# Kernel tuning notes

Measured on AMD Instinct MI355X. Metric: run time of the kernel, lower is better.

Reference implementation:

```python
import jax, jax.numpy as jnp
import numpy as np


def setup_inputs() -> dict:
    key = jax.random.key(0)
    ks = jax.random.split(key, 8)
    B, T, C = 4, 1024, 1024
    s = 1.0 / np.sqrt(C)
    return {
        "q": jax.random.normal(ks[0], (B, T, C), jnp.float32),
        "k": jax.random.normal(ks[1], (B, T, C), jnp.float32),
        "v": jax.random.normal(ks[2], (B, T, C), jnp.float32),
        "Wq": jax.random.normal(ks[3], (C, C), jnp.float32) * s,
        "Wk": jax.random.normal(ks[4], (C, C), jnp.float32) * s,
        "Wv": jax.random.normal(ks[5], (C, C), jnp.float32) * s,
        "Wp": jax.random.normal(ks[6], (C, C), jnp.float32) * s,
        "bp": jnp.zeros((C,), jnp.float32),
        "n_head": 16,
        "kernel_size": 16,
    }


def reference(q, k, v, Wq, Wk, Wv, Wp, bp, n_head, kernel_size):
    B, T, C = q.shape
    H = n_head
    D = C // H

    def split_heads(x, W):
        # nn.Linear applies x @ W.T
        return (x @ W.T).reshape(B, T, H, D).transpose(0, 2, 1, 3)  # (B,H,T,D)

    qp = split_heads(q, Wq)
    kp = split_heads(k, Wk)
    vp = split_heads(v, Wv)

    # Faithful to the torch double loop: wei[b,h,i,j] = sum over feature dims
    # d in [max(0, j-ks), min(T, j+ks)) (clipped to [0,D)) of qp[b,h,i,d]*kp[b,h,i,d] / sqrt(D).
    # Both windows index sequence position i; the window slides over the head_dim axis.
    p = qp * kp / jnp.sqrt(jnp.asarray(D, qp.dtype))          # (B,H,T,D)
    cs = jnp.cumsum(p, axis=-1)
    cs = jnp.concatenate([jnp.zeros(cs.shape[:-1] + (1,), cs.dtype), cs], axis=-1)  # (B,H,T,D+1)
    j = jnp.arange(T)
    start = jnp.clip(j - kernel_size, 0, D)                   # (T,)
    end = jnp.clip(jnp.minimum(j + kernel_size, T), 0, D)     # (T,)
    wei = cs[..., end] - cs[..., start]                       # (B,H,T,T): windowed partial dot of row i

    attn = jax.nn.softmax(wei, axis=-1)
    out = jnp.einsum("bhts,bhsd->bhtd", attn, vp)             # (B,H,T,D)
    out = out.transpose(0, 2, 1, 3).reshape(B, T, C)
    out = out @ Wp.T + bp
    # dropout is identity in eval mode
    return out
```

## Files before the change

### kernel.cpp

```cpp
#include <hip/hip_runtime.h>
#include <hip/hip_bf16.h>
#include <stdint.h>


typedef __bf16 bf16x8 __attribute__((ext_vector_type(8)));
typedef float f32x4 __attribute__((ext_vector_type(4)));

#define AS1(p) ((__attribute__((address_space(1))) void*)(p))
#define AS3(p) ((__attribute__((address_space(3))) void*)(p))

__global__ __launch_bounds__(256) void cvt_kernel(
    const float* __restrict__ s0, const float* __restrict__ s1,
    const float* __restrict__ s2, const float* __restrict__ s3,
    ushort4* __restrict__ dst, int n4)
{
  const float* s = blockIdx.y == 0 ? s0 : blockIdx.y == 1 ? s1
                 : blockIdx.y == 2 ? s2 : s3;
  int i = blockIdx.x * 256 + threadIdx.x;
  if (i >= n4) return;
  float4 v = ((const float4*)s)[i];
  union { ushort4 u; __hip_bfloat16 h[4]; } c;
  c.h[0] = __float2bfloat16(v.x); c.h[1] = __float2bfloat16(v.y);
  c.h[2] = __float2bfloat16(v.z); c.h[3] = __float2bfloat16(v.w);
  dst[(size_t)blockIdx.y * n4 + i] = c.u;
}

template <typename OutT>
__device__ __forceinline__ void gemm_bt_body(
    const __hip_bfloat16* __restrict__ A, const __hip_bfloat16* __restrict__ Bw,
    OutT* __restrict__ C, const float* __restrict__ bias, int mBase, int nBase)
{
  const int N = 1024, K = 1024;
  __shared__ __align__(16) __hip_bfloat16 As[128 * 32];
  __shared__ __align__(16) __hip_bfloat16 Bs[128 * 32];
  const int t = threadIdx.x;
  const int wv = t >> 6, lane = t & 63;
  const int wRow = (wv >> 1) * 64, wCol = (wv & 1) * 64;
  const int mrow = lane & 15, kq = lane >> 4;

  f32x4 acc[4][4] = {};

  for (int k0 = 0; k0 < K; k0 += 32) {
    __syncthreads();
#pragma unroll
    for (int tI = 0; tI < 2; ++tI) {
      int chunk = wv * 2 + tI;
      int byteOff = chunk * 1024 + lane * 16;
      int row = byteOff >> 6;
      int colEl = (byteOff & 63) >> 1;
      const __hip_bfloat16* ga = A + (size_t)(mBase + row) * K + k0 + colEl;
      __builtin_amdgcn_global_load_lds(AS1((void*)ga), AS3(&As[chunk * 512]), 16, 0, 0);
      const __hip_bfloat16* gb = Bw + (size_t)(nBase + row) * K + k0 + colEl;
      __builtin_amdgcn_global_load_lds(AS1((void*)gb), AS3(&Bs[chunk * 512]), 16, 0, 0);
    }
    __syncthreads();

    bf16x8 af[4], bf[4];
#pragma unroll
    for (int mi = 0; mi < 4; ++mi)
      af[mi] = *(const bf16x8*)&As[(wRow + mi * 16 + mrow) * 32 + kq * 8];
#pragma unroll
    for (int ni = 0; ni < 4; ++ni)
      bf[ni] = *(const bf16x8*)&Bs[(wCol + ni * 16 + mrow) * 32 + kq * 8];
#pragma unroll
    for (int mi = 0; mi < 4; ++mi)
#pragma unroll
      for (int ni = 0; ni < 4; ++ni)
        acc[mi][ni] = __builtin_amdgcn_mfma_f32_16x16x32_bf16(af[mi], bf[ni], acc[mi][ni], 0, 0, 0);
  }

#pragma unroll
  for (int mi = 0; mi < 4; ++mi)
#pragma unroll
    for (int ni = 0; ni < 4; ++ni)
#pragma unroll
      for (int r = 0; r < 4; ++r) {
        int row = mBase + wRow + mi * 16 + kq * 4 + r;
        int col = nBase + wCol + ni * 16 + mrow;
        float v = acc[mi][ni][r];
        if (bias) v += bias[col];
        if constexpr (__is_same(OutT, __hip_bfloat16))
          C[(size_t)row * N + col] = __float2bfloat16(v);
        else
          C[(size_t)row * N + col] = v;
      }
}

__global__ __launch_bounds__(256) void qkv_gemm_kernel(
    const __hip_bfloat16* __restrict__ Xbf, const __hip_bfloat16* __restrict__ Wbf,
    __hip_bfloat16* __restrict__ OutP)
{
  int l = blockIdx.x;
  int mm = l % 96;
  int z = mm >> 5, m = mm & 31, n = l / 96;
  gemm_bt_body<__hip_bfloat16>(Xbf + (size_t)z * 4194304, Wbf + (size_t)z * 1048576,
                               OutP + (size_t)z * 4194304, nullptr, m * 128, n * 128);
}

__global__ __launch_bounds__(256) void final_gemm_kernel(
    const __hip_bfloat16* __restrict__ Abf, const __hip_bfloat16* __restrict__ Wpbf,
    float* __restrict__ Out, const float* __restrict__ bias)
{
  int l = blockIdx.x;
  int m = l & 31, n = l >> 5;
  gemm_bt_body<float>(Abf, Wpbf, Out, bias, m * 128, n * 128);
}

__global__ __launch_bounds__(256) void tail_partial_kernel(
    const __hip_bfloat16* __restrict__ VP, float* __restrict__ partial)
{
  const int seg = blockIdx.x, bh = blockIdx.y;
  const int b = bh >> 4, h = bh & 15;
  const int d = threadIdx.x & 63, wv = threadIdx.x >> 6;
  const int jBase = 80 + seg * 59;
  float s = 0.0f;
  for (int r = wv; r < 59; r += 4)
    s += __bfloat162float(VP[((size_t)(b * 1024 + jBase + r)) * 1024 + h * 64 + d]);
  __shared__ float red[4][64];
  red[wv][d] = s;
  __syncthreads();
  if (threadIdx.x < 64)
    partial[(bh * 16 + seg) * 64 + threadIdx.x] =
        red[0][threadIdx.x] + red[1][threadIdx.x] + red[2][threadIdx.x] + red[3][threadIdx.x];
}

__global__ __launch_bounds__(256) void attn_kernel(
    const __hip_bfloat16* __restrict__ QP, const __hip_bfloat16* __restrict__ KP,
    const __hip_bfloat16* __restrict__ VP, const float* __restrict__ partial,
    __hip_bfloat16* __restrict__ OUTA)
{
  const int b = blockIdx.z, h = blockIdx.y, i0 = blockIdx.x * 64;
  const int t = threadIdx.x, lane = t & 63, wv = t >> 6;

  __shared__ float csl[64][65];
  __shared__ __align__(16) __hip_bfloat16 wlb[64][96];
  __shared__ __align__(16) __hip_bfloat16 vpt[64][104];
  __shared__ float scl[64], tlw[64], tail[64];

  if (t < 64) {
    const float* pp = partial + (b * 16 + h) * 16 * 64 + t;
    float s = 0.0f;
#pragma unroll
    for (int seg = 0; seg < 16; ++seg) s += pp[seg * 64];
    tail[t] = s;
  }

  for (int idx = t; idx < 80 * 64; idx += 256) {
    int j = idx >> 6, d = idx & 63;
    vpt[d][j] = VP[((size_t)(b * 1024 + j)) * 1024 + h * 64 + d];
  }
  for (int idx = t; idx < 64 * 16; idx += 256) {
    int d = idx >> 4, j = 80 + (idx & 15);
    vpt[d][j] = __float2bfloat16(0.0f);
  }

  for (int ii = 0; ii < 16; ++ii) {
    int i = wv * 16 + ii;
    size_t row = ((size_t)(b * 1024 + i0 + i)) * 1024 + h * 64 + lane;
    float p = __bfloat162float(QP[row]) * __bfloat162float(KP[row]) * 0.125f;
#pragma unroll
    for (int delta = 1; delta < 64; delta <<= 1) {
      float up = __shfl_up(p, (unsigned)delta, 64);
      if (lane >= delta) p += up;
    }
    csl[i][lane] = p;
  }
  __syncthreads();

  {
    int i = t >> 2, jg = t & 3;
    float wloc[20];
    float mx = 0.0f;
#pragma unroll
    for (int q = 0; q < 20; ++q) {
      int j = jg + 4 * q;
      int s = j - 16; s = s < 0 ? 0 : s;
      int e = j + 16; e = e > 64 ? 64 : e;
      float w = csl[i][e - 1] - (s > 0 ? csl[i][s - 1] : 0.0f);
      wloc[q] = w;
      mx = fmaxf(mx, w);
    }
    mx = fmaxf(mx, __shfl_xor(mx, 1, 64));
    mx = fmaxf(mx, __shfl_xor(mx, 2, 64));
    float sum = 0.0f;
#pragma unroll
    for (int q = 0; q < 20; ++q) {
      float e_ = __expf(wloc[q] - mx);
      wlb[i][jg + 4 * q] = __float2bfloat16(e_);
      sum += e_;
    }
#pragma unroll
    for (int q = 0; q < 4; ++q)
      wlb[i][80 + jg + 4 * q] = __float2bfloat16(0.0f);
    sum += __shfl_xor(sum, 1, 64);
    sum += __shfl_xor(sum, 2, 64);
    float tw = __expf(-mx);
    sum += 944.0f * tw;
    if (jg == 0) { scl[i] = 1.0f / sum; tlw[i] = tw / sum; }
  }
  __syncthreads();

  {
    const int mh = (wv >> 1) * 32, nh = (wv & 1) * 32;
    const int mrow = lane & 15, kq = lane >> 4;
    f32x4 acc[2][2] = {};
#pragma unroll
    for (int k0 = 0; k0 < 96; k0 += 32) {
      bf16x8 af[2], bf[2];
#pragma unroll
      for (int mi = 0; mi < 2; ++mi)
        af[mi] = *(const bf16x8*)&wlb[mh + mi * 16 + mrow][k0 + kq * 8];
#pragma unroll
      for (int ni = 0; ni < 2; ++ni)
        bf[ni] = *(const bf16x8*)&vpt[nh + ni * 16 + mrow][k0 + kq * 8];
#pragma unroll
      for (int mi = 0; mi < 2; ++mi)
#pragma unroll
        for (int ni = 0; ni < 2; ++ni)
          acc[mi][ni] = __builtin_amdgcn_mfma_f32_16x16x32_bf16(af[mi], bf[ni], acc[mi][ni], 0, 0, 0);
    }
#pragma unroll
    for (int mi = 0; mi < 2; ++mi)
#pragma unroll
      for (int ni = 0; ni < 2; ++ni)
#pragma unroll
        for (int r = 0; r < 4; ++r) {
          int i = mh + mi * 16 + kq * 4 + r;
          int d = nh + ni * 16 + mrow;
          float o = acc[mi][ni][r] * scl[i] + tlw[i] * tail[d];
          OUTA[((size_t)(b * 1024 + i0 + i)) * 1024 + h * 64 + d] = __float2bfloat16(o);
        }
  }
}

extern "C" void kernel_launch(void* const* d_in, const int* in_sizes, int n_in,
                              void* d_out, int out_size, void* d_ws, size_t ws_size,
                              hipStream_t stream)
{
  (void)in_sizes; (void)n_in; (void)out_size; (void)ws_size;
  const float* q  = (const float*)d_in[0];
  const float* k  = (const float*)d_in[1];
  const float* v  = (const float*)d_in[2];
  const float* Wq = (const float*)d_in[3];
  const float* Wk = (const float*)d_in[4];
  const float* Wv = (const float*)d_in[5];
  const float* Wp = (const float*)d_in[6];
  const float* bp = (const float*)d_in[7];

  char* ws = (char*)d_ws;
  __hip_bfloat16* qkv_bf = (__hip_bfloat16*)(ws);
  __hip_bfloat16* w_bf   = (__hip_bfloat16*)(ws + 25165824);
  __hip_bfloat16* QKVpb  = (__hip_bfloat16*)(ws + 33554432);
  __hip_bfloat16* OUTA   = (__hip_bfloat16*)(ws + 58720256);
  float* partial = (float*)(ws);
  float* out = (float*)d_out;

  cvt_kernel<<<dim3(4096, 3, 1), 256, 0, stream>>>(q, k, v, q, (ushort4*)qkv_bf, 1048576);
  cvt_kernel<<<dim3(1024, 4, 1), 256, 0, stream>>>(Wq, Wk, Wv, Wp, (ushort4*)w_bf, 262144);
  qkv_gemm_kernel<<<dim3(768), 256, 0, stream>>>(qkv_bf, w_bf, QKVpb);
  tail_partial_kernel<<<dim3(16, 64), 256, 0, stream>>>(QKVpb + (size_t)2 * 4194304, partial);
  attn_kernel<<<dim3(16, 16, 4), 256, 0, stream>>>(QKVpb, QKVpb + 4194304,
                                                   QKVpb + (size_t)2 * 4194304, partial, OUTA);
  final_gemm_kernel<<<dim3(256), 256, 0, stream>>>(OUTA, w_bf + (size_t)3 * 1048576, out, bp);
}
```

Before: 204.5 us.

## Project only first 128 V rows and compute tail sum via linearity

Instead of projecting all 1024 V rows through Wv, only the first 128 rows per batch go through the GEMM. The tail sum of projected V over rows 80 onward is computed as Wv applied to the raw fp32 V row sum, using a column-sum kernel plus a small GEMV. The two conversion launches are merged into one, and the GEMM tiles get pre-offset base pointers. This removes about a third of the QKV GEMM work, but the fp32 tail path now reads the full fp32 V, and the tail sum rounds differently from the previous bf16 path.

After: 234.0 us. 14.4% more time.

```diff
diff --git a/kernel.cpp b/kernel.cpp
--- a/kernel.cpp
+++ b/kernel.cpp
@@ -10,25 +10,39 @@
 #define AS3(p) ((__attribute__((address_space(3))) void*)(p))
 
 __global__ __launch_bounds__(256) void cvt_kernel(
-    const float* __restrict__ s0, const float* __restrict__ s1,
-    const float* __restrict__ s2, const float* __restrict__ s3,
-    ushort4* __restrict__ dst, int n4)
-{
-  const float* s = blockIdx.y == 0 ? s0 : blockIdx.y == 1 ? s1
-                 : blockIdx.y == 2 ? s2 : s3;
+    const float* __restrict__ q, const float* __restrict__ k,
+    const float* __restrict__ v, const float* __restrict__ Wq,
+    const float* __restrict__ Wk, const float* __restrict__ Wv,
+    const float* __restrict__ Wp,
+    ushort4* __restrict__ qk_bf, ushort4* __restrict__ w_bf,
+    ushort4* __restrict__ vhead_bf)
+{
+  const int y = blockIdx.y;
   int i = blockIdx.x * 256 + threadIdx.x;
-  if (i >= n4) return;
-  float4 v = ((const float4*)s)[i];
+  const float* src; ushort4* dst; int n4; size_t srcIdx;
+  if (y < 2) {
+    n4 = 1048576; if (i >= n4) return;
+    src = y == 0 ? q : k; dst = qk_bf + (size_t)y * 1048576; srcIdx = i;
+  } else if (y < 6) {
+    n4 = 262144; if (i >= n4) return;
+    src = y == 2 ? Wq : y == 3 ? Wk : y == 4 ? Wv : Wp;
+    dst = w_bf + (size_t)(y - 2) * 262144; srcIdx = i;
+  } else {
+    n4 = 131072; if (i >= n4) return;
+    int b = i >> 15, rem = i & 32767;
+    src = v; dst = vhead_bf; srcIdx = (size_t)b * 262144 + rem;
+  }
+  float4 val = ((const float4*)src)[srcIdx];
   union { ushort4 u; __hip_bfloat16 h[4]; } c;
-  c.h[0] = __float2bfloat16(v.x); c.h[1] = __float2bfloat16(v.y);
-  c.h[2] = __float2bfloat16(v.z); c.h[3] = __float2bfloat16(v.w);
-  dst[(size_t)blockIdx.y * n4 + i] = c.u;
+  c.h[0] = __float2bfloat16(val.x); c.h[1] = __float2bfloat16(val.y);
+  c.h[2] = __float2bfloat16(val.z); c.h[3] = __float2bfloat16(val.w);
+  dst[i] = c.u;
 }
 
 template <typename OutT>
-__device__ __forceinline__ void gemm_bt_body(
+__device__ __forceinline__ void gemm_tile(
     const __hip_bfloat16* __restrict__ A, const __hip_bfloat16* __restrict__ Bw,
-    OutT* __restrict__ C, const float* __restrict__ bias, int mBase, int nBase)
+    OutT* __restrict__ C, const float* __restrict__ bias)
 {
   const int N = 1024, K = 1024;
   __shared__ __align__(16) __hip_bfloat16 As[128 * 32];
@@ -48,9 +62,9 @@
       int byteOff = chunk * 1024 + lane * 16;
       int row = byteOff >> 6;
       int colEl = (byteOff & 63) >> 1;
-      const __hip_bfloat16* ga = A + (size_t)(mBase + row) * K + k0 + colEl;
+      const __hip_bfloat16* ga = A + (size_t)row * K + k0 + colEl;
       __builtin_amdgcn_global_load_lds(AS1((void*)ga), AS3(&As[chunk * 512]), 16, 0, 0);
-      const __hip_bfloat16* gb = Bw + (size_t)(nBase + row) * K + k0 + colEl;
+      const __hip_bfloat16* gb = Bw + (size_t)row * K + k0 + colEl;
       __builtin_amdgcn_global_load_lds(AS1((void*)gb), AS3(&Bs[chunk * 512]), 16, 0, 0);
     }
     __syncthreads();
@@ -75,58 +89,90 @@
     for (int ni = 0; ni < 4; ++ni)
 #pragma unroll
       for (int r = 0; r < 4; ++r) {
-        int row = mBase + wRow + mi * 16 + kq * 4 + r;
-        int col = nBase + wCol + ni * 16 + mrow;
-        float v = acc[mi][ni][r];
-        if (bias) v += bias[col];
+        int row = wRow + mi * 16 + kq * 4 + r;
+        int col = wCol + ni * 16 + mrow;
+        float val = acc[mi][ni][r];
+        if (bias) val += bias[col];
         if constexpr (__is_same(OutT, __hip_bfloat16))
-          C[(size_t)row * N + col] = __float2bfloat16(v);
+          C[(size_t)row * N + col] = __float2bfloat16(val);
         else
-          C[(size_t)row * N + col] = v;
+          C[(size_t)row * N + col] = val;
       }
 }
 
 __global__ __launch_bounds__(256) void qkv_gemm_kernel(
-    const __hip_bfloat16* __restrict__ Xbf, const __hip_bfloat16* __restrict__ Wbf,
-    __hip_bfloat16* __restrict__ OutP)
+    const __hip_bfloat16* __restrict__ QKbf, const __hip_bfloat16* __restrict__ Wbf,
+    const __hip_bfloat16* __restrict__ Vhead,
+    __hip_bfloat16* __restrict__ QKp, __hip_bfloat16* __restrict__ VPh)
 {
   int l = blockIdx.x;
-  int mm = l % 96;
-  int z = mm >> 5, m = mm & 31, n = l / 96;
-  gemm_bt_body<__hip_bfloat16>(Xbf + (size_t)z * 4194304, Wbf + (size_t)z * 1048576,
-                               OutP + (size_t)z * 4194304, nullptr, m * 128, n * 128);
+  if (l < 512) {
+    int zm = l & 63, z = zm >> 5, m = zm & 31, n = l >> 6;
+    gemm_tile<__hip_bfloat16>(
+        QKbf + (size_t)z * 4194304 + (size_t)m * 131072,
+        Wbf + (size_t)z * 1048576 + (size_t)n * 131072,
+        QKp + (size_t)z * 4194304 + (size_t)m * 131072 + n * 128, nullptr);
+  } else {
+    int vb = l - 512, b = vb >> 3, n = vb & 7;
+    gemm_tile<__hip_bfloat16>(
+        Vhead + (size_t)b * 131072,
+        Wbf + (size_t)2 * 1048576 + (size_t)n * 131072,
+        VPh + (size_t)b * 131072 + n * 128, nullptr);
+  }
 }
 
 __global__ __launch_bounds__(256) void final_gemm_kernel(
     const __hip_bfloat16* __restrict__ Abf, const __hip_bfloat16* __restrict__ Wpbf,
     float* __restrict__ Out, const float* __restrict__ bias)
 {
-  int l = blockIdx.x;
-  int m = l & 31, n = l >> 5;
-  gemm_bt_body<float>(Abf, Wpbf, Out, bias, m * 128, n * 128);
-}
-
-__global__ __launch_bounds__(256) void tail_partial_kernel(
-    const __hip_bfloat16* __restrict__ VP, float* __restrict__ partial)
-{
-  const int seg = blockIdx.x, bh = blockIdx.y;
-  const int b = bh >> 4, h = bh & 15;
-  const int d = threadIdx.x & 63, wv = threadIdx.x >> 6;
-  const int jBase = 80 + seg * 59;
+  int l = blockIdx.x, m = l & 31, n = l >> 5;
+  gemm_tile<float>(Abf + (size_t)m * 131072, Wpbf + (size_t)n * 131072,
+                   Out + (size_t)m * 131072 + n * 128, bias + n * 128);
+}
+
+__global__ __launch_bounds__(256) void vsum_kernel(
+    const float* __restrict__ v, float* __restrict__ partialv)
+{
+  const int cseg = blockIdx.x, jseg = blockIdx.y, b = blockIdx.z;
+  const int c = cseg * 256 + threadIdx.x;
+  const int jBase = 80 + jseg * 118;
   float s = 0.0f;
-  for (int r = wv; r < 59; r += 4)
-    s += __bfloat162float(VP[((size_t)(b * 1024 + jBase + r)) * 1024 + h * 64 + d]);
-  __shared__ float red[4][64];
-  red[wv][d] = s;
+  for (int r = 0; r < 118; ++r)
+    s += v[((size_t)(b * 1024 + jBase + r)) * 1024 + c];
+  partialv[(size_t)(b * 8 + jseg) * 1024 + c] = s;
+}
+
+__global__ __launch_bounds__(256) void tails_kernel(
+    const float* __restrict__ partialv, const float* __restrict__ Wv,
+    float* __restrict__ tails)
+{
+  const int bc = blockIdx.x, b = bc >> 4, cseg = bc & 15;
+  const int t = threadIdx.x, cl = t >> 2, kq = t & 3;
+  __shared__ float vs[1024];
+  for (int idx = t; idx < 1024; idx += 256) {
+    float s = 0.0f;
+#pragma unroll
+    for (int j = 0; j < 8; ++j) s += partialv[(size_t)(b * 8 + j) * 1024 + idx];
+    vs[idx] = s;
+  }
   __syncthreads();
-  if (threadIdx.x < 64)
-    partial[(bh * 16 + seg) * 64 + threadIdx.x] =
-        red[0][threadIdx.x] + red[1][threadIdx.x] + red[2][threadIdx.x] + red[3][threadIdx.x];
+  const int c = cseg * 64 + cl;
+  const float4* wr = (const float4*)(Wv + (size_t)c * 1024);
+  const float4* vs4 = (const float4*)vs;
+  float acc = 0.0f;
+  for (int kk = 0; kk < 64; ++kk) {
+    float4 w4 = wr[kq * 64 + kk];
+    float4 s4 = vs4[kq * 64 + kk];
+    acc += w4.x * s4.x + w4.y * s4.y + w4.z * s4.z + w4.w * s4.w;
+  }
+  acc += __shfl_xor(acc, 1, 64);
+  acc += __shfl_xor(acc, 2, 64);
+  if (kq == 0) tails[(size_t)b * 1024 + c] = acc;
 }
 
 __global__ __launch_bounds__(256) void attn_kernel(
     const __hip_bfloat16* __restrict__ QP, const __hip_bfloat16* __restrict__ KP,
-    const __hip_bfloat16* __restrict__ VP, const float* __restrict__ partial,
+    const __hip_bfloat16* __restrict__ VPh, const float* __restrict__ tails,
     __hip_bfloat16* __restrict__ OUTA)
 {
   const int b = blockIdx.z, h = blockIdx.y, i0 = blockIdx.x * 64;
@@ -137,17 +183,11 @@
   __shared__ __align__(16) __hip_bfloat16 vpt[64][104];
   __shared__ float scl[64], tlw[64], tail[64];
 
-  if (t < 64) {
-    const float* pp = partial + (b * 16 + h) * 16 * 64 + t;
-    float s = 0.0f;
-#pragma unroll
-    for (int seg = 0; seg < 16; ++seg) s += pp[seg * 64];
-    tail[t] = s;
-  }
+  if (t < 64) tail[t] = tails[(size_t)b * 1024 + h * 64 + t];
 
   for (int idx = t; idx < 80 * 64; idx += 256) {
     int j = idx >> 6, d = idx & 63;
-    vpt[d][j] = VP[((size_t)(b * 1024 + j)) * 1024 + h * 64 + d];
+    vpt[d][j] = VPh[((size_t)(b * 128 + j)) * 1024 + h * 64 + d];
   }
   for (int idx = t; idx < 64 * 16; idx += 256) {
     int d = idx >> 4, j = 80 + (idx & 15);
@@ -248,18 +288,23 @@
   const float* bp = (const float*)d_in[7];
 
   char* ws = (char*)d_ws;
-  __hip_bfloat16* qkv_bf = (__hip_bfloat16*)(ws);
-  __hip_bfloat16* w_bf   = (__hip_bfloat16*)(ws + 25165824);
-  __hip_bfloat16* QKVpb  = (__hip_bfloat16*)(ws + 33554432);
-  __hip_bfloat16* OUTA   = (__hip_bfloat16*)(ws + 58720256);
-  float* partial = (float*)(ws);
+  __hip_bfloat16* qk_bf    = (__hip_bfloat16*)(ws);
+  __hip_bfloat16* w_bf     = (__hip_bfloat16*)(ws + 16777216);
+  __hip_bfloat16* vhead_bf = (__hip_bfloat16*)(ws + 25165824);
+  float*          partialv = (float*)(ws + 26214400);
+  float*          tails    = (float*)(ws + 26345472);
+  __hip_bfloat16* QKp      = (__hip_bfloat16*)(ws + 27262976);
+  __hip_bfloat16* VPh      = (__hip_bfloat16*)(ws + 44040192);
+  __hip_bfloat16* OUTA     = (__hip_bfloat16*)(ws + 45088768);
   float* out = (float*)d_out;
 
-  cvt_kernel<<<dim3(4096, 3, 1), 256, 0, stream>>>(q, k, v, q, (ushort4*)qkv_bf, 1048576);
-  cvt_kernel<<<dim3(1024, 4, 1), 256, 0, stream>>>(Wq, Wk, Wv, Wp, (ushort4*)w_bf, 262144);
-  qkv_gemm_kernel<<<dim3(768), 256, 0, stream>>>(qkv_bf, w_bf, QKVpb);
-  tail_partial_kernel<<<dim3(16, 64), 256, 0, stream>>>(QKVpb + (size_t)2 * 4194304, partial);
-  attn_kernel<<<dim3(16, 16, 4), 256, 0, stream>>>(QKVpb, QKVpb + 4194304,
-                                                   QKVpb + (size_t)2 * 4194304, partial, OUTA);
-  final_gemm_kernel<<<dim3(256), 256, 0, stream>>>(OUTA, w_bf + (size_t)3 * 1048576, out, bp);
-}
+  cvt_kernel<<<dim3(4096, 7), 256, 0, stream>>>(q, k, v, Wq, Wk, Wv, Wp,
+      (ushort4*)qk_bf, (ushort4*)w_bf, (ushort4*)vhead_bf);
+  qkv_gemm_kernel<<<dim3(544), 256, 0, stream>>>(qk_bf, w_bf, vhead_bf, QKp, VPh);
+  vsum_kernel<<<dim3(4, 8, 4), 256, 0, stream>>>(v, partialv);
+  tails_kernel<<<dim3(64), 256, 0, stream>>>(partialv, Wv, tails);
+  attn_kernel<<<dim3(16, 16, 4), 256, 0, stream>>>(QKp, QKp + (size_t)4194304,
+                                                   VPh, tails, OUTA);
+  final_gemm_kernel<<<dim3(256), 256, 0, stream>>>(OUTA, w_bf + (size_t)3 * 1048576,
+                                                   out, bp);
+}
```

## Merge conversion launches, deepen GEMM K-step, split final GEMM into 64-row tiles

Applied to the files above, without the earlier changes.

Folds the two fp32-to-bf16 conversion launches into one kernel covering activations and weights. The shared GEMM body now stages 64 K-elements per iteration in two LDS halves, which halves the number of barrier pairs. The final projection GEMM becomes a dedicated 64x128-tile kernel with 512 blocks instead of 256, to spread work across more CUs. The trade-off is more LDS per block, which can lower occupancy, and a less even load-issue pattern in the final kernel.

Result: faster. 187.4 us (-8.4%).

```diff
diff --git a/kernel.cpp b/kernel.cpp
--- a/kernel.cpp
+++ b/kernel.cpp
@@ -10,29 +10,38 @@
 #define AS3(p) ((__attribute__((address_space(3))) void*)(p))
 
 __global__ __launch_bounds__(256) void cvt_kernel(
-    const float* __restrict__ s0, const float* __restrict__ s1,
-    const float* __restrict__ s2, const float* __restrict__ s3,
-    ushort4* __restrict__ dst, int n4)
-{
-  const float* s = blockIdx.y == 0 ? s0 : blockIdx.y == 1 ? s1
-                 : blockIdx.y == 2 ? s2 : s3;
-  int i = blockIdx.x * 256 + threadIdx.x;
-  if (i >= n4) return;
-  float4 v = ((const float4*)s)[i];
+    const float* __restrict__ q, const float* __restrict__ k,
+    const float* __restrict__ v, const float* __restrict__ Wq,
+    const float* __restrict__ Wk, const float* __restrict__ Wv,
+    const float* __restrict__ Wp,
+    ushort4* __restrict__ qkv_bf, ushort4* __restrict__ w_bf)
+{
+  int idx = blockIdx.x * 256 + threadIdx.x;
+  const float* src; ushort4* dst; int i;
+  if (idx < 3145728) {
+    int which = idx >> 20; i = idx & 1048575;
+    src = which == 0 ? q : which == 1 ? k : v;
+    dst = qkv_bf + (size_t)which * 1048576 + i;
+  } else {
+    int w = idx - 3145728; int which = w >> 18; i = w & 262143;
+    src = which == 0 ? Wq : which == 1 ? Wk : which == 2 ? Wv : Wp;
+    dst = w_bf + w;
+  }
+  float4 val = ((const float4*)src)[i];
   union { ushort4 u; __hip_bfloat16 h[4]; } c;
-  c.h[0] = __float2bfloat16(v.x); c.h[1] = __float2bfloat16(v.y);
-  c.h[2] = __float2bfloat16(v.z); c.h[3] = __float2bfloat16(v.w);
-  dst[(size_t)blockIdx.y * n4 + i] = c.u;
+  c.h[0] = __float2bfloat16(val.x); c.h[1] = __float2bfloat16(val.y);
+  c.h[2] = __float2bfloat16(val.z); c.h[3] = __float2bfloat16(val.w);
+  dst[0] = c.u;
 }
 
 template <typename OutT>
-__device__ __forceinline__ void gemm_bt_body(
+__device__ __forceinline__ void gemm_tile128(
     const __hip_bfloat16* __restrict__ A, const __hip_bfloat16* __restrict__ Bw,
-    OutT* __restrict__ C, const float* __restrict__ bias, int mBase, int nBase)
+    OutT* __restrict__ C, const float* __restrict__ bias)
 {
   const int N = 1024, K = 1024;
-  __shared__ __align__(16) __hip_bfloat16 As[128 * 32];
-  __shared__ __align__(16) __hip_bfloat16 Bs[128 * 32];
+  __shared__ __align__(16) __hip_bfloat16 As[2][128 * 32];
+  __shared__ __align__(16) __hip_bfloat16 Bs[2][128 * 32];
   const int t = threadIdx.x;
   const int wv = t >> 6, lane = t & 63;
   const int wRow = (wv >> 1) * 64, wCol = (wv & 1) * 64;
@@ -40,70 +49,139 @@
 
   f32x4 acc[4][4] = {};
 
-  for (int k0 = 0; k0 < K; k0 += 32) {
+  for (int k0 = 0; k0 < K; k0 += 64) {
     __syncthreads();
 #pragma unroll
-    for (int tI = 0; tI < 2; ++tI) {
-      int chunk = wv * 2 + tI;
-      int byteOff = chunk * 1024 + lane * 16;
-      int row = byteOff >> 6;
-      int colEl = (byteOff & 63) >> 1;
-      const __hip_bfloat16* ga = A + (size_t)(mBase + row) * K + k0 + colEl;
-      __builtin_amdgcn_global_load_lds(AS1((void*)ga), AS3(&As[chunk * 512]), 16, 0, 0);
-      const __hip_bfloat16* gb = Bw + (size_t)(nBase + row) * K + k0 + colEl;
-      __builtin_amdgcn_global_load_lds(AS1((void*)gb), AS3(&Bs[chunk * 512]), 16, 0, 0);
-    }
+    for (int half = 0; half < 2; ++half)
+#pragma unroll
+      for (int tI = 0; tI < 2; ++tI) {
+        int chunk = wv * 2 + tI;
+        int byteOff = chunk * 1024 + lane * 16;
+        int row = byteOff >> 6;
+        int colEl = (byteOff & 63) >> 1;
+        const __hip_bfloat16* ga = A + (size_t)row * K + k0 + half * 32 + colEl;
+        __builtin_amdgcn_global_load_lds(AS1((void*)ga), AS3(&As[half][chunk * 512]), 16, 0, 0);
+        const __hip_bfloat16* gb = Bw + (size_t)row * K + k0 + half * 32 + colEl;
+        __builtin_amdgcn_global_load_lds(AS1((void*)gb), AS3(&Bs[half][chunk * 512]), 16, 0, 0);
+      }
     __syncthreads();
 
-    bf16x8 af[4], bf[4];
-#pragma unroll
-    for (int mi = 0; mi < 4; ++mi)
-      af[mi] = *(const bf16x8*)&As[(wRow + mi * 16 + mrow) * 32 + kq * 8];
+#pragma unroll
+    for (int half = 0; half < 2; ++half) {
+      bf16x8 af[4], bf[4];
+#pragma unroll
+      for (int mi = 0; mi < 4; ++mi)
+        af[mi] = *(const bf16x8*)&As[half][(wRow + mi * 16 + mrow) * 32 + kq * 8];
+#pragma unroll
+      for (int ni = 0; ni < 4; ++ni)
+        bf[ni] = *(const bf16x8*)&Bs[half][(wCol + ni * 16 + mrow) * 32 + kq * 8];
+#pragma unroll
+      for (int mi = 0; mi < 4; ++mi)
+#pragma unroll
+        for (int ni = 0; ni < 4; ++ni)
+          acc[mi][ni] = __builtin_amdgcn_mfma_f32_16x16x32_bf16(af[mi], bf[ni], acc[mi][ni], 0, 0, 0);
+    }
+  }
+
+#pragma unroll
+  for (int mi = 0; mi < 4; ++mi)
 #pragma unroll
     for (int ni = 0; ni < 4; ++ni)
-      bf[ni] = *(const bf16x8*)&Bs[(wCol + ni * 16 + mrow) * 32 + kq * 8];
-#pragma unroll
-    for (int mi = 0; mi < 4; ++mi)
-#pragma unroll
-      for (int ni = 0; ni < 4; ++ni)
-        acc[mi][ni] = __builtin_amdgcn_mfma_f32_16x16x32_bf16(af[mi], bf[ni], acc[mi][ni], 0, 0, 0);
-  }
-
-#pragma unroll
-  for (int mi = 0; mi < 4; ++mi)
-#pragma unroll
-    for (int ni = 0; ni < 4; ++ni)
 #pragma unroll
       for (int r = 0; r < 4; ++r) {
-        int row = mBase + wRow + mi * 16 + kq * 4 + r;
-        int col = nBase + wCol + ni * 16 + mrow;
-        float v = acc[mi][ni][r];
-        if (bias) v += bias[col];
+        int row = wRow + mi * 16 + kq * 4 + r;
+        int col = wCol + ni * 16 + mrow;
+        float val = acc[mi][ni][r];
+        if (bias) val += bias[col];
         if constexpr (__is_same(OutT, __hip_bfloat16))
-          C[(size_t)row * N + col] = __float2bfloat16(v);
+          C[(size_t)row * N + col] = __float2bfloat16(val);
         else
-          C[(size_t)row * N + col] = v;
+          C[(size_t)row * N + col] = val;
       }
 }
 
 __global__ __launch_bounds__(256) void qkv_gemm_kernel(
-    const __hip_bfloat16* __restrict__ Xbf, const __hip_bfloat16* __restrict__ Wbf,
-    __hip_bfloat16* __restrict__ OutP)
+    const __hip_bfloat16* __restrict__ QKVbf, const __hip_bfloat16* __restrict__ Wbf,
+    __hip_bfloat16* __restrict__ QKVp)
 {
   int l = blockIdx.x;
-  int mm = l % 96;
-  int z = mm >> 5, m = mm & 31, n = l / 96;
-  gemm_bt_body<__hip_bfloat16>(Xbf + (size_t)z * 4194304, Wbf + (size_t)z * 1048576,
-                               OutP + (size_t)z * 4194304, nullptr, m * 128, n * 128);
+  int n = l / 96, mm = l % 96, z = mm >> 5, m = mm & 31;
+  gemm_tile128<__hip_bfloat16>(
+      QKVbf + (size_t)z * 4194304 + (size_t)m * 131072,
+      Wbf + (size_t)z * 1048576 + (size_t)n * 131072,
+      QKVp + (size_t)z * 4194304 + (size_t)m * 131072 + n * 128, nullptr);
 }
 
 __global__ __launch_bounds__(256) void final_gemm_kernel(
     const __hip_bfloat16* __restrict__ Abf, const __hip_bfloat16* __restrict__ Wpbf,
-    float* __restrict__ Out, const float* __restrict__ bias)
-{
+    float* __restrict__ Out, const float* __restrict__ biasAll)
+{
+  const int N = 1024, K = 1024;
   int l = blockIdx.x;
-  int m = l & 31, n = l >> 5;
-  gemm_bt_body<float>(Abf, Wpbf, Out, bias, m * 128, n * 128);
+  int m = l & 63, n = l >> 6;
+  const __hip_bfloat16* A = Abf + (size_t)m * 65536;
+  const __hip_bfloat16* Bw = Wpbf + (size_t)n * 131072;
+  float* C = Out + (size_t)m * 65536 + n * 128;
+  const float* bias = biasAll + n * 128;
+
+  __shared__ __align__(16) __hip_bfloat16 As[2][64 * 32];
+  __shared__ __align__(16) __hip_bfloat16 Bs[2][128 * 32];
+  const int t = threadIdx.x;
+  const int wv = t >> 6, lane = t & 63;
+  const int wRow = (wv >> 1) * 32, wCol = (wv & 1) * 64;
+  const int mrow = lane & 15, kq = lane >> 4;
+
+  f32x4 acc[2][4] = {};
+
+  for (int k0 = 0; k0 < K; k0 += 64) {
+    __syncthreads();
+#pragma unroll
+    for (int tI = 0; tI < 6; ++tI) {
+      int c = wv * 6 + tI;
+      int byteOff, row, colEl;
+      if (c < 8) {
+        int half = c >> 2, ch = c & 3;
+        byteOff = ch * 1024 + lane * 16;
+        row = byteOff >> 6; colEl = (byteOff & 63) >> 1;
+        const __hip_bfloat16* ga = A + (size_t)row * K + k0 + half * 32 + colEl;
+        __builtin_amdgcn_global_load_lds(AS1((void*)ga), AS3(&As[half][ch * 512]), 16, 0, 0);
+      } else {
+        int cb = c - 8, half = cb >> 3, ch = cb & 7;
+        byteOff = ch * 1024 + lane * 16;
+        row = byteOff >> 6; colEl = (byteOff & 63) >> 1;
+        const __hip_bfloat16* gb = Bw + (size_t)row * K + k0 + half * 32 + colEl;
+        __builtin_amdgcn_global_load_lds(AS1((void*)gb), AS3(&Bs[half][ch * 512]), 16, 0, 0);
+      }
+    }
+    __syncthreads();
+
+#pragma unroll
+    for (int half = 0; half < 2; ++half) {
+      bf16x8 af[2], bf[4];
+#pragma unroll
+      for (int mi = 0; mi < 2; ++mi)
+        af[mi] = *(const bf16x8*)&As[half][(wRow + mi * 16 + mrow) * 32 + kq * 8];
+#pragma unroll
+      for (int ni = 0; ni < 4; ++ni)
+        bf[ni] = *(const bf16x8*)&Bs[half][(wCol + ni * 16 + mrow) * 32 + kq * 8];
+#pragma unroll
+      for (int mi = 0; mi < 2; ++mi)
+#pragma unroll
+        for (int ni = 0; ni < 4; ++ni)
+          acc[mi][ni] = __builtin_amdgcn_mfma_f32_16x16x32_bf16(af[mi], bf[ni], acc[mi][ni], 0, 0, 0);
+    }
+  }
+
+#pragma unroll
+  for (int mi = 0; mi < 2; ++mi)
+#pragma unroll
+    for (int ni = 0; ni < 4; ++ni)
+#pragma unroll
+      for (int r = 0; r < 4; ++r) {
+        int row = wRow + mi * 16 + kq * 4 + r;
+        int col = wCol + ni * 16 + mrow;
+        C[(size_t)row * N + col] = acc[mi][ni][r] + bias[col];
+      }
 }
 
 __global__ __launch_bounds__(256) void tail_partial_kernel(
@@ -250,16 +328,17 @@
   char* ws = (char*)d_ws;
   __hip_bfloat16* qkv_bf = (__hip_bfloat16*)(ws);
   __hip_bfloat16* w_bf   = (__hip_bfloat16*)(ws + 25165824);
-  __hip_bfloat16* QKVpb  = (__hip_bfloat16*)(ws + 33554432);
+  __hip_bfloat16* QKVp   = (__hip_bfloat16*)(ws + 33554432);
   __hip_bfloat16* OUTA   = (__hip_bfloat16*)(ws + 58720256);
   float* partial = (float*)(ws);
   float* out = (float*)d_out;
 
-  cvt_kernel<<<dim3(4096, 3, 1), 256, 0, stream>>>(q, k, v, q, (ushort4*)qkv_bf, 1048576);
-  cvt_kernel<<<dim3(1024, 4, 1), 256, 0, stream>>>(Wq, Wk, Wv, Wp, (ushort4*)w_bf, 262144);
-  qkv_gemm_kernel<<<dim3(768), 256, 0, stream>>>(qkv_bf, w_bf, QKVpb);
-  tail_partial_kernel<<<dim3(16, 64), 256, 0, stream>>>(QKVpb + (size_t)2 * 4194304, partial);
-  attn_kernel<<<dim3(16, 16, 4), 256, 0, stream>>>(QKVpb, QKVpb + 4194304,
-                                                   QKVpb + (size_t)2 * 4194304, partial, OUTA);
-  final_gemm_kernel<<<dim3(256), 256, 0, stream>>>(OUTA, w_bf + (size_t)3 * 1048576, out, bp);
-}
+  cvt_kernel<<<dim3(16384), 256, 0, stream>>>(q, k, v, Wq, Wk, Wv, Wp,
+      (ushort4*)qkv_bf, (ushort4*)w_bf);
+  qkv_gemm_kernel<<<dim3(768), 256, 0, stream>>>(qkv_bf, w_bf, QKVp);
+  tail_partial_kernel<<<dim3(16, 64), 256, 0, stream>>>(QKVp + (size_t)2 * 4194304, partial);
+  attn_kernel<<<dim3(16, 16, 4), 256, 0, stream>>>(QKVp, QKVp + (size_t)4194304,
+                                                   QKVp + (size_t)2 * 4194304, partial, OUTA);
+  final_gemm_kernel<<<dim3(512), 256, 0, stream>>>(OUTA, w_bf + (size_t)3 * 1048576,
+                                                   out, bp);
+}
```
